# Kernel tuning notes

Measured on AMD Instinct MI355X. Metric: run time of the kernel, lower is better.

## Reference

```python
import jax, jax.numpy as jnp
import numpy as np

B, S, H, E, K = 4, 2048, 1024, 8, 2


def setup_inputs() -> dict:
    key = jax.random.key(0)
    k0, k1, k2 = jax.random.split(key, 3)
    x = jax.random.normal(k0, (B, S, H), dtype=jnp.float32)
    # gate: Linear(H -> E); torch stores W as [out,in], we keep [E,H]
    gate_w = jax.random.normal(k1, (E, H), dtype=jnp.float32) * 0.02
    gate_b = jnp.zeros((E,), dtype=jnp.float32)
    # experts: E x Linear(H -> H); stored as [E, H_in, H_out]
    expert_w = jax.random.normal(k2, (E, H, H), dtype=jnp.float32) * 0.02
    expert_b = jnp.zeros((E, H), dtype=jnp.float32)
    return {"x": x, "gate_w": gate_w, "gate_b": gate_b,
            "expert_w": expert_w, "expert_b": expert_b}


def reference(x, gate_w, gate_b, expert_w, expert_b):
    bsz, seq_len, h = x.shape
    xt = x.reshape(-1, h)                      # [T, H]
    T = xt.shape[0]

    # router (moe_router): softmax -> top-k -> renormalize
    logits = xt @ gate_w.T + gate_b            # [T, E]
    routing_probs = jax.nn.softmax(logits, axis=-1)
    top_k_probs, top_k_index = jax.lax.top_k(routing_probs, K)
    top_k_probs = top_k_probs / jnp.sum(top_k_probs, axis=1, keepdims=True)
    top_k_probs = top_k_probs.astype(x.dtype)

    # combine weights: scatter normalized top-k probs into [T, E]
    rows = jnp.arange(T)[:, None]
    combine = jnp.zeros((T, E), dtype=x.dtype).at[rows, top_k_index].add(top_k_probs)

    # per-expert FFN over all tokens, then weighted combine
    # (equivalent math to the gather / index_add loop: zero weights contribute zero)
    y = jnp.einsum('th,eho->teo', xt, expert_w) + expert_b[None, :, :]  # [T, E, H]
    out = jnp.einsum('te,teh->th', combine, y)                          # [T, H]

    final_output = out.reshape(bsz, seq_len, h)
    return final_output, top_k_index, routing_probs
```

## Files before the change

### kernel.cpp

```cpp
#include <hip/hip_runtime.h>
#include <hip/hip_bf16.h>
#include <stdint.h>

typedef unsigned short ushort_t;
typedef __bf16 bf16x8 __attribute__((ext_vector_type(8)));
typedef float f32x4 __attribute__((ext_vector_type(4)));

#define T_TOK 8192
#define H_DIM 1024
#define E_EXP 8
#define BM 256
#define BN 256
#define BK 64
#define NKT (H_DIM / BK)
#define NITER (NKT / 2)
#define NWG_G 512

#define CNT_STRIDE 64
#define RTOK 32
#define RBLOCKS (T_TOK / RTOK)
#define TP_BLOCKS ((H_DIM / 32) * (H_DIM / 32) * E_EXP)

static __device__ __forceinline__ ushort_t f2bf(float f) {
  union { float f; uint32_t u; } c; c.f = f;
  uint32_t u = c.u;
  uint32_t r = u + 0x7FFFu + ((u >> 16) & 1u);
  return (ushort_t)(r >> 16);
}

__global__ __launch_bounds__(256) void router_transpose(
    const float* __restrict__ x, const float* __restrict__ gw,
    const float* __restrict__ gb, const float* __restrict__ ew,
    float* __restrict__ out_idx, float* __restrict__ out_probs,
    ushort_t* __restrict__ x_bf, int* __restrict__ counts,
    int* __restrict__ tok, float* __restrict__ wts, int* __restrict__ slotmap,
    ushort_t* __restrict__ wT)
{
  __shared__ int   sm_eid[RTOK * 2];
  __shared__ float sm_wt[RTOK * 2];
  __shared__ int   lcnt[E_EXP], lbase[E_EXP], lpos[E_EXP];
  __shared__ float tile[32][33];

  const int tid = threadIdx.x;

  if (blockIdx.x >= RBLOCKS) {
    const int tb = blockIdx.x - RBLOCKS;
    const int e = tb >> 10;
    const int n0 = (tb & 31) * 32, k0 = ((tb >> 5) & 31) * 32;
    const float* we = ew + (size_t)e * H_DIM * H_DIM;
    ushort_t* wTe = wT + (size_t)e * H_DIM * H_DIM;
    const int tx = tid & 31, ty = tid >> 5;
#pragma unroll
    for (int i = 0; i < 4; i++)
      tile[ty + 8 * i][tx] = we[(size_t)(k0 + ty + 8 * i) * H_DIM + n0 + tx];
    __syncthreads();
#pragma unroll
    for (int i = 0; i < 4; i++)
      wTe[(size_t)(n0 + ty + 8 * i) * H_DIM + k0 + tx] = f2bf(tile[tx][ty + 8 * i]);
    return;
  }

  const int wave = tid >> 6, l = tid & 63;
  if (tid < E_EXP) { lcnt[tid] = 0; lpos[tid] = 0; }
  __syncthreads();

  const int t0 = blockIdx.x * RTOK;
  for (int it = 0; it < RTOK / 4; it++) {
    const int lt = wave * (RTOK / 4) + it;
    const int t = t0 + lt;
    const float* xt = x + (size_t)t * H_DIM;
    float acc[E_EXP];
#pragma unroll
    for (int e = 0; e < E_EXP; e++) acc[e] = 0.f;
#pragma unroll
    for (int i = 0; i < 4; i++) {
      const int h = (i * 64 + l) * 4;
      const float4 xv = *reinterpret_cast<const float4*>(xt + h);
      ushort4 b;
      b.x = f2bf(xv.x); b.y = f2bf(xv.y); b.z = f2bf(xv.z); b.w = f2bf(xv.w);
      *reinterpret_cast<ushort4*>(x_bf + (size_t)t * H_DIM + h) = b;
#pragma unroll
      for (int e = 0; e < E_EXP; e++) {
        const float4 g = *reinterpret_cast<const float4*>(gw + e * H_DIM + h);
        acc[e] += xv.x * g.x + xv.y * g.y + xv.z * g.z + xv.w * g.w;
      }
    }
#pragma unroll
    for (int e = 0; e < E_EXP; e++) {
      float v = acc[e];
#pragma unroll
      for (int off = 32; off; off >>= 1) v += __shfl_xor(v, off);
      acc[e] = v;
    }
    if (l == 0) {
      float lg[E_EXP], pb[E_EXP];
      float m = -1e30f;
#pragma unroll
      for (int e = 0; e < E_EXP; e++) { lg[e] = acc[e] + gb[e]; m = fmaxf(m, lg[e]); }
      float s = 0.f;
#pragma unroll
      for (int e = 0; e < E_EXP; e++) { pb[e] = expf(lg[e] - m); s += pb[e]; }
      const float inv = 1.f / s;
#pragma unroll
      for (int e = 0; e < E_EXP; e++) {
        pb[e] *= inv;
        out_probs[(size_t)t * E_EXP + e] = pb[e];
      }
      int i0 = 0; float p0 = pb[0];
#pragma unroll
      for (int e = 1; e < E_EXP; e++) if (pb[e] > p0) { p0 = pb[e]; i0 = e; }
      int i1 = -1; float p1 = -1.f;
#pragma unroll
      for (int e = 0; e < E_EXP; e++) if (e != i0 && pb[e] > p1) { p1 = pb[e]; i1 = e; }
      out_idx[(size_t)t * 2 + 0] = (float)i0;
      out_idx[(size_t)t * 2 + 1] = (float)i1;
      const float rn = 1.f / (p0 + p1);
      sm_eid[lt * 2 + 0] = i0; sm_wt[lt * 2 + 0] = p0 * rn;
      sm_eid[lt * 2 + 1] = i1; sm_wt[lt * 2 + 1] = p1 * rn;
    }
  }
  __syncthreads();

  if (tid < RTOK * 2) atomicAdd(&lcnt[sm_eid[tid]], 1);
  __syncthreads();
  if (tid < E_EXP) lbase[tid] = atomicAdd(&counts[tid * CNT_STRIDE], lcnt[tid]);
  __syncthreads();
  if (tid < RTOK * 2) {
    const int e = sm_eid[tid];
    const int p = lbase[e] + atomicAdd(&lpos[e], 1);
    tok[e * T_TOK + p] = t0 + (tid >> 1);
    wts[e * T_TOK + p] = sm_wt[tid];
    slotmap[(t0 + (tid >> 1)) * 2 + (tid & 1)] = e * T_TOK + p;
  }
}

#define GLDS16(gp, lp)                                                         \
  __builtin_amdgcn_global_load_lds(                                            \
      (const __attribute__((address_space(1))) void*)(gp),                     \
      (__attribute__((address_space(3))) void*)(lp), 16, 0, 0)

#define WAITV6() asm volatile("s_waitcnt vmcnt(6)" ::: "memory")
#define WAITV0() asm volatile("s_waitcnt vmcnt(0)" ::: "memory")
#define LGKM0()                                                                \
  do {                                                                         \
    asm volatile("s_waitcnt lgkmcnt(0)" ::: "memory");                         \
    __builtin_amdgcn_sched_barrier(0);                                         \
  } while (0)
#define BAR()                                                                  \
  do {                                                                         \
    __builtin_amdgcn_sched_barrier(0);                                         \
    __builtin_amdgcn_s_barrier();                                              \
    __builtin_amdgcn_sched_barrier(0);                                         \
  } while (0)

__global__ __launch_bounds__(512, 2) void moe_gemm(
    const ushort_t* __restrict__ x_bf, const ushort_t* __restrict__ wT,
    const float* __restrict__ bias, const int* __restrict__ counts,
    const int* __restrict__ tok, const float* __restrict__ wts,
    ushort_t* __restrict__ y)
{
  __shared__ __align__(16) ushort_t AsR[2 * 2 * BM * 32];
  __shared__ __align__(16) ushort_t BsR[2 * 2 * BM * 32];
  __shared__ int stok[BM];
  __shared__ float swt[BM];
#define AS_(buf, kh, idx) AsR[((buf) * 2 + (kh)) * 8192 + (idx)]
#define BS_(buf, kh, idx) BsR[((buf) * 2 + (kh)) * 8192 + (idx)]

  const int tid = threadIdx.x;
  const int bid = blockIdx.x;

  int ne[E_EXP], fl[E_EXP];
  int bulk_total = 0;
#pragma unroll
  for (int i = 0; i < E_EXP; i++) {
    ne[i] = counts[i * CNT_STRIDE];
    fl[i] = ne[i] >> 8;
    bulk_total += fl[i] * 4;
  }

  if (bid < bulk_total) {
    int e = 0, local = bid, done = 0;
#pragma unroll
    for (int i = 0; i < E_EXP; i++) {
      const int sz = fl[i] * 4;
      if (!done) { if (local < sz) { e = i; done = 1; } else local -= sz; }
    }
    const int mt = local >> 2;
    const int nt = local & 3;

    if (tid < BM) {
      stok[tid] = tok[e * T_TOK + mt * BM + tid];
      swt[tid] = wts[e * T_TOK + mt * BM + tid];
    }
    __syncthreads();

    const int r0 = tid >> 2;
    const int cp = (tid & 3) ^ ((tid >> 3) & 3);
    const ushort_t* wTe = wT + (size_t)e * H_DIM * H_DIM;
    const ushort_t* aP0 = x_bf + (size_t)stok[r0] * H_DIM + cp * 8;
    const ushort_t* aP1 = x_bf + (size_t)stok[r0 + 128] * H_DIM + cp * 8;
    const ushort_t* bP0 = wTe + (size_t)(nt * BN + r0) * H_DIM + cp * 8;
    const ushort_t* bP1 = wTe + (size_t)(nt * BN + r0 + 128) * H_DIM + cp * 8;
    const int d0 = tid * 8;
    const int d1 = (tid + 512) * 8;

#define STAGE_A(t, kh, buf)                                                    \
  do {                                                                         \
    GLDS16(aP0 + (t) * BK + (kh) * 32, &AS_((buf), (kh), d0));                 \
    GLDS16(aP1 + (t) * BK + (kh) * 32, &AS_((buf), (kh), d1));                 \
  } while (0)
#define STAGE_B(t, kh, buf)                                                    \
  do {                                                                         \
    GLDS16(bP0 + (t) * BK + (kh) * 32, &BS_((buf), (kh), d0));                 \
    GLDS16(bP1 + (t) * BK + (kh) * 32, &BS_((buf), (kh), d1));                 \
  } while (0)

    const int l = tid & 63;
    const int wid = tid >> 6;
    const int wm = wid >> 2, wn = wid & 3;
    const int fr = l & 15;
    const int g = l >> 4;
    const int sl = g ^ ((l >> 1) & 3);
    const int arow0 = wm * 128 + fr;
    const int brow0 = wn * 64 + fr;

    bf16x8 af[8], bv[2];
    f32x4 acc[8][4] = {};

#define READ_A(buf, kk)                                                        \
  do {                                                                         \
    _Pragma("unroll") for (int mi = 0; mi < 8; mi++)                           \
        af[mi] = *reinterpret_cast<const bf16x8*>(                             \
            &AS_((buf), (kk), (arow0 + mi * 16) * 32 + sl * 8));               \
  } while (0)
#define READ_B(buf, kk, nh)                                                    \
  do {                                                                         \
    _Pragma("unroll") for (int j = 0; j < 2; j++)                              \
        bv[j] = *reinterpret_cast<const bf16x8*>(                              \
            &BS_((buf), (kk), (brow0 + ((nh) * 2 + j) * 16) * 32 + sl * 8));   \
  } while (0)
#define MFMA16(nh)                                                             \
  do {                                                                         \
    __builtin_amdgcn_s_setprio(1);                                             \
    _Pragma("unroll") for (int mi = 0; mi < 8; mi++)                           \
        _Pragma("unroll") for (int j = 0; j < 2; j++)                          \
            acc[mi][(nh) * 2 + j] = __builtin_amdgcn_mfma_f32_16x16x32_bf16(   \
                af[mi], bv[j], acc[mi][(nh) * 2 + j], 0, 0, 0);                \
    __builtin_amdgcn_s_setprio(0);                                             \
  } while (0)

#define ITER_BODY(TT, MORE)                                                    \
  do {                                                                         \
                                                                       \
    READ_A(0, 0); READ_B(0, 0, 0);                                             \
    STAGE_B((TT) + 1, 1, 1);                                                   \
    BAR(); LGKM0(); MFMA16(0); BAR();                                          \
                                                                       \
    READ_B(0, 0, 1);                                                           \
    if (MORE) STAGE_A((TT) + 2, 0, 0);                                         \
    BAR(); LGKM0(); MFMA16(1); BAR();                                          \
                                                                       \
    READ_A(0, 1); READ_B(0, 1, 0);                                             \
    if (MORE) STAGE_B((TT) + 2, 0, 0);                                         \
    BAR(); LGKM0(); MFMA16(0); BAR();                                          \
                                               \
    READ_B(0, 1, 1);                                                           \
    if (MORE) { STAGE_A((TT) + 2, 1, 0); WAITV6(); } else { WAITV0(); }        \
    BAR(); LGKM0(); MFMA16(1); BAR();                                          \
                                                                       \
    READ_A(1, 0); READ_B(1, 0, 0);                                             \
    if (MORE) STAGE_B((TT) + 2, 1, 0);                                         \
    BAR(); LGKM0(); MFMA16(0); BAR();                                          \
                                                                       \
    READ_B(1, 0, 1);                                                           \
    if (MORE) STAGE_A((TT) + 3, 0, 1);                                         \
    BAR(); LGKM0(); MFMA16(1); BAR();                                          \
                                                                       \
    READ_A(1, 1); READ_B(1, 1, 0);                                             \
    if (MORE) STAGE_B((TT) + 3, 0, 1);                                         \
    BAR(); LGKM0(); MFMA16(0); BAR();                                          \
                                               \
    READ_B(1, 1, 1);                                                           \
    if (MORE) { STAGE_A((TT) + 3, 1, 1); WAITV6(); }                           \
    BAR(); LGKM0(); MFMA16(1); BAR();                                          \
  } while (0)

    STAGE_A(0, 0, 0); STAGE_B(0, 0, 0); STAGE_A(0, 1, 0); STAGE_B(0, 1, 0);
    STAGE_A(1, 0, 1); STAGE_B(1, 0, 1); STAGE_A(1, 1, 1);
    WAITV6();
    BAR();

#pragma unroll 1
    for (int it = 0; it < NITER - 1; ++it) {
      const int t = 2 * it;
      ITER_BODY(t, 1);
    }
    {
      const int t = 2 * (NITER - 1);
      ITER_BODY(t, 0);
    }

    ushort_t* ye = y + ((size_t)e * T_TOK + (size_t)mt * BM) * H_DIM;
    float bias4[4];
#pragma unroll
    for (int nj = 0; nj < 4; nj++)
      bias4[nj] = bias[e * H_DIM + nt * BN + wn * 64 + nj * 16 + fr];
#pragma unroll
    for (int mi = 0; mi < 8; mi++) {
      const int rr0 = wm * 128 + mi * 16 + g * 4;
#pragma unroll
      for (int r = 0; r < 4; r++) {
        const int row = rr0 + r;
        const float wgt = swt[row];
#pragma unroll
        for (int nj = 0; nj < 4; nj++) {
          const int n = nt * BN + wn * 64 + nj * 16 + fr;
          ye[(size_t)row * H_DIM + n] = f2bf(wgt * (acc[mi][nj][r] + bias4[nj]));
        }
      }
    }
    return;
  }

  {
    const int tb0 = bid - bulk_total;
    int tc[E_EXP];
    int tail_total = 0;
#pragma unroll
    for (int i = 0; i < E_EXP; i++) {
      const int rem = ne[i] - (fl[i] << 8);
      tc[i] = (rem + 63) >> 6;
      tail_total += tc[i] * 8;
    }
    if (tb0 >= tail_total) return;
    int e = 0, local = tb0, done = 0;
#pragma unroll
    for (int i = 0; i < E_EXP; i++) {
      const int sz = tc[i] * 8;
      if (!done) { if (local < sz) { e = i; done = 1; } else local -= sz; }
    }
    const int mtt = local >> 3;
    const int ntt = local & 7;
    const int row0 = (fl[e] << 8) + mtt * 64;
    int valid = ne[e] - row0; if (valid > 64) valid = 64;

    if (tid < 64) {
      int slot = row0 + tid;
      if (slot >= ne[e]) slot = ne[e] - 1;
      stok[tid] = tok[e * T_TOK + slot];
      swt[tid] = wts[e * T_TOK + slot];
    }
    __syncthreads();

    const ushort_t* wTe = wT + (size_t)e * H_DIM * H_DIM;
    const int trow = tid >> 3;
    const int tlc = (tid & 7) ^ (trow & 7);
    const ushort_t* taS = x_bf + (size_t)stok[trow] * H_DIM + tlc * 8;
    const ushort_t* tbS0 = wTe + (size_t)(ntt * 128 + trow) * H_DIM + tlc * 8;
    const ushort_t* tbS1 = tbS0 + (size_t)64 * H_DIM;

#define TSTAGE(t, buf)                                                         \
  do {                                                                         \
    GLDS16(taS + (t) * BK, &AsR[(buf) * 4096 + tid * 8]);                      \
    GLDS16(tbS0 + (t) * BK, &BsR[(buf) * 8192 + tid * 8]);                     \
    GLDS16(tbS1 + (t) * BK, &BsR[(buf) * 8192 + (tid + 512) * 8]);             \
  } while (0)

    const int l = tid & 63;
    const int wid = tid >> 6;
    const int fr = l & 15;
    const int g = l >> 4;
    const int tph0 = (g ^ (fr & 7)) * 8;
    const int tph1 = ((4 ^ g) ^ (fr & 7)) * 8;

    f32x4 tacc[4] = {};

    TSTAGE(0, 0);
    WAITV0();
    BAR();

#pragma unroll
    for (int t = 0; t < NKT; ++t) {
      if (t + 1 < NKT) TSTAGE(t + 1, (t + 1) & 1);
      const ushort_t* Ab = &AsR[(t & 1) * 4096];
      const ushort_t* Bb = &BsR[(t & 1) * 8192];
#pragma unroll
      for (int kk = 0; kk < 2; kk++) {
        const int ph = kk ? tph1 : tph0;
        const bf16x8 tbv = *reinterpret_cast<const bf16x8*>(
            &Bb[(wid * 16 + fr) * 64 + ph]);
#pragma unroll
        for (int mi = 0; mi < 4; mi++) {
          const bf16x8 tav = *reinterpret_cast<const bf16x8*>(
              &Ab[(mi * 16 + fr) * 64 + ph]);
          tacc[mi] = __builtin_amdgcn_mfma_f32_16x16x32_bf16(
              tav, tbv, tacc[mi], 0, 0, 0);
        }
      }
      WAITV0();
      BAR();
    }

    ushort_t* ye = y + ((size_t)e * T_TOK + row0) * H_DIM;
    const int ncol = ntt * 128 + wid * 16 + fr;
    const float bs = bias[e * H_DIM + ncol];
#pragma unroll
    for (int mi = 0; mi < 4; mi++) {
      const int rb = mi * 16 + g * 4;
#pragma unroll
      for (int r = 0; r < 4; r++) {
        const int row = rb + r;
        if (row < valid) {
          ye[(size_t)row * H_DIM + ncol] = f2bf(swt[row] * (tacc[mi][r] + bs));
        }
      }
    }
  }
}

__global__ __launch_bounds__(256) void combine_kernel(
    const ushort_t* __restrict__ y, const int* __restrict__ slotmap,
    float* __restrict__ out)
{
  const int t = blockIdx.x;
  const int s0 = slotmap[t * 2 + 0];
  const int s1 = slotmap[t * 2 + 1];
  const ushort_t* r0 = y + (size_t)s0 * H_DIM;
  const ushort_t* r1 = y + (size_t)s1 * H_DIM;
  float* o = out + (size_t)t * H_DIM;
  const int h = threadIdx.x * 4;
  const ushort4 u0 = *reinterpret_cast<const ushort4*>(r0 + h);
  const ushort4 u1 = *reinterpret_cast<const ushort4*>(r1 + h);
  float4 v;
  union { uint32_t u; float f; } c;
  c.u = (uint32_t)u0.x << 16; v.x = c.f; c.u = (uint32_t)u1.x << 16; v.x += c.f;
  c.u = (uint32_t)u0.y << 16; v.y = c.f; c.u = (uint32_t)u1.y << 16; v.y += c.f;
  c.u = (uint32_t)u0.z << 16; v.z = c.f; c.u = (uint32_t)u1.z << 16; v.z += c.f;
  c.u = (uint32_t)u0.w << 16; v.w = c.f; c.u = (uint32_t)u1.w << 16; v.w += c.f;
  *reinterpret_cast<float4*>(o + h) = v;
}

extern "C" void kernel_launch(void* const* d_in, const int* in_sizes, int n_in,
                              void* d_out, int out_size, void* d_ws, size_t ws_size,
                              hipStream_t stream)
{
  const float* x  = (const float*)d_in[0];
  const float* gw = (const float*)d_in[1];
  const float* gb = (const float*)d_in[2];
  const float* ew = (const float*)d_in[3];
  const float* eb = (const float*)d_in[4];

  float* out = (float*)d_out;
  float* out_final = out;
  float* out_idx   = out + (size_t)T_TOK * H_DIM;
  float* out_probs = out_idx + (size_t)T_TOK * 2;

  char* ws = (char*)d_ws;
  size_t off = 0;
  int*      counts  = (int*)(ws + off); off += 4096;
  int*      tok     = (int*)(ws + off); off += (size_t)E_EXP * T_TOK * 4;
  float*    wts     = (float*)(ws + off); off += (size_t)E_EXP * T_TOK * 4;
  int*      slotmap = (int*)(ws + off); off += (size_t)T_TOK * 2 * 4;
  ushort_t* x_bf    = (ushort_t*)(ws + off); off += (size_t)T_TOK * H_DIM * 2;
  ushort_t* wT      = (ushort_t*)(ws + off); off += (size_t)E_EXP * H_DIM * H_DIM * 2;
  ushort_t* y       = (ushort_t*)(ws + off); off += (size_t)E_EXP * T_TOK * H_DIM * 2;

  hipMemsetAsync(counts, 0, 4096, stream);

  router_transpose<<<RBLOCKS + TP_BLOCKS, 256, 0, stream>>>(
      x, gw, gb, ew, out_idx, out_probs, x_bf, counts, tok, wts, slotmap, wT);
  moe_gemm<<<NWG_G, 512, 0, stream>>>(x_bf, wT, eb, counts, tok, wts, y);
  combine_kernel<<<T_TOK, 256, 0, stream>>>(y, slotmap, out_final);
}
```

Baseline: 97.30 us.

## Switch MoE GEMM to persistent workgroups with XCD-affine atomic work queues

Replaces the static one-tile-per-workgroup grid with a persistent kernel of 256 workgroups that pull tiles from per-expert atomic counters, preferring the expert matching their XCD index so each expert's weights stay in one XCD's L2. Once those queues drain, workgroups steal from other experts and then take tail tiles from a shared counter. This targets load imbalance and L2 locality for weight reads. The cost is extra atomics and barriers per tile, and the queue counters in the counts buffer must be zeroed before each launch; that reset is not visible here.

Result: slower. 126.2 us (+29.7%).

```diff
diff --git a/kernel.cpp b/kernel.cpp
--- a/kernel.cpp
+++ b/kernel.cpp
@@ -14,7 +14,7 @@
 #define BK 64
 #define NKT (H_DIM / BK)
 #define NITER (NKT / 2)
-#define NWG_G 512
+#define NWG_G 256
 
 #define CNT_STRIDE 64
 #define RTOK 32
@@ -155,7 +155,7 @@
 
 __global__ __launch_bounds__(512, 2) void moe_gemm(
     const ushort_t* __restrict__ x_bf, const ushort_t* __restrict__ wT,
-    const float* __restrict__ bias, const int* __restrict__ counts,
+    const float* __restrict__ bias, int* __restrict__ counts,
     const int* __restrict__ tok, const float* __restrict__ wts,
     ushort_t* __restrict__ y)
 {
@@ -163,46 +163,71 @@
   __shared__ __align__(16) ushort_t BsR[2 * 2 * BM * 32];
   __shared__ int stok[BM];
   __shared__ float swt[BM];
+  __shared__ int s_q, s_e, s_kind;
 #define AS_(buf, kh, idx) AsR[((buf) * 2 + (kh)) * 8192 + (idx)]
 #define BS_(buf, kh, idx) BsR[((buf) * 2 + (kh)) * 8192 + (idx)]
 
   const int tid = threadIdx.x;
-  const int bid = blockIdx.x;
-
-  int ne[E_EXP], fl[E_EXP];
-  int bulk_total = 0;
+  const int xcd = blockIdx.x & 7;
+
+  int ne[E_EXP], fl[E_EXP], tc[E_EXP];
+  int tail_total = 0;
 #pragma unroll
   for (int i = 0; i < E_EXP; i++) {
     ne[i] = counts[i * CNT_STRIDE];
     fl[i] = ne[i] >> 8;
-    bulk_total += fl[i] * 4;
+    tc[i] = ((ne[i] - (fl[i] << 8)) + 63) >> 6;
+    tail_total += tc[i] * 8;
   }
-
-  if (bid < bulk_total) {
-    int e = 0, local = bid, done = 0;
-#pragma unroll
-    for (int i = 0; i < E_EXP; i++) {
-      const int sz = fl[i] * 4;
-      if (!done) { if (local < sz) { e = i; done = 1; } else local -= sz; }
-    }
-    const int mt = local >> 2;
-    const int nt = local & 3;
-
-    if (tid < BM) {
-      stok[tid] = tok[e * T_TOK + mt * BM + tid];
-      swt[tid] = wts[e * T_TOK + mt * BM + tid];
+  int* qb = counts + 512;
+  int* qt = counts + 512 + 8 * 16;
+
+  const int l = tid & 63;
+  const int wid = tid >> 6;
+  const int fr = l & 15;
+  const int g = l >> 4;
+
+  for (;;) {
+    __syncthreads();
+    if (tid == 0) {
+      int q = -1, te = -1, kind = 0;
+      for (int dx = 0; dx < E_EXP && q < 0; ++dx) {
+        const int x2 = (xcd + dx) & 7;
+        const int lim = fl[x2] * 4;
+        if (lim > 0) {
+          const int c = atomicAdd(&qb[x2 * 16], 1);
+          if (c < lim) { q = c; te = x2; }
+        }
+      }
+      if (q < 0) {
+        const int c = atomicAdd(qt, 1);
+        if (c < tail_total) { q = c; kind = 1; }
+      }
+      s_q = q; s_e = te; s_kind = kind;
     }
     __syncthreads();
-
-    const int r0 = tid >> 2;
-    const int cp = (tid & 3) ^ ((tid >> 3) & 3);
-    const ushort_t* wTe = wT + (size_t)e * H_DIM * H_DIM;
-    const ushort_t* aP0 = x_bf + (size_t)stok[r0] * H_DIM + cp * 8;
-    const ushort_t* aP1 = x_bf + (size_t)stok[r0 + 128] * H_DIM + cp * 8;
-    const ushort_t* bP0 = wTe + (size_t)(nt * BN + r0) * H_DIM + cp * 8;
-    const ushort_t* bP1 = wTe + (size_t)(nt * BN + r0 + 128) * H_DIM + cp * 8;
-    const int d0 = tid * 8;
-    const int d1 = (tid + 512) * 8;
+    if (s_q < 0) break;
+
+    if (s_kind == 0) {
+      const int e = s_e;
+      const int mt = s_q >> 2;
+      const int nt = s_q & 3;
+
+      if (tid < BM) {
+        stok[tid] = tok[e * T_TOK + mt * BM + tid];
+        swt[tid] = wts[e * T_TOK + mt * BM + tid];
+      }
+      __syncthreads();
+
+      const int r0 = tid >> 2;
+      const int cp = (tid & 3) ^ ((tid >> 3) & 3);
+      const ushort_t* wTe = wT + (size_t)e * H_DIM * H_DIM;
+      const ushort_t* aP0 = x_bf + (size_t)stok[r0] * H_DIM + cp * 8;
+      const ushort_t* aP1 = x_bf + (size_t)stok[r0 + 128] * H_DIM + cp * 8;
+      const ushort_t* bP0 = wTe + (size_t)(nt * BN + r0) * H_DIM + cp * 8;
+      const ushort_t* bP1 = wTe + (size_t)(nt * BN + r0 + 128) * H_DIM + cp * 8;
+      const int d0 = tid * 8;
+      const int d1 = (tid + 512) * 8;
 
 #define STAGE_A(t, kh, buf)                                                    \
   do {                                                                         \
@@ -215,17 +240,13 @@
     GLDS16(bP1 + (t) * BK + (kh) * 32, &BS_((buf), (kh), d1));                 \
   } while (0)
 
-    const int l = tid & 63;
-    const int wid = tid >> 6;
-    const int wm = wid >> 2, wn = wid & 3;
-    const int fr = l & 15;
-    const int g = l >> 4;
-    const int sl = g ^ ((l >> 1) & 3);
-    const int arow0 = wm * 128 + fr;
-    const int brow0 = wn * 64 + fr;
-
-    bf16x8 af[8], bv[2];
-    f32x4 acc[8][4] = {};
+      const int wm = wid >> 2, wn = wid & 3;
+      const int sl = g ^ ((l >> 1) & 3);
+      const int arow0 = wm * 128 + fr;
+      const int brow0 = wn * 64 + fr;
+
+      bf16x8 af[8], bv[2];
+      f32x4 acc[8][4] = {};
 
 #define READ_A(buf, kk)                                                        \
   do {                                                                         \
@@ -285,79 +306,66 @@
     BAR(); LGKM0(); MFMA16(1); BAR();                                          \
   } while (0)
 
-    STAGE_A(0, 0, 0); STAGE_B(0, 0, 0); STAGE_A(0, 1, 0); STAGE_B(0, 1, 0);
-    STAGE_A(1, 0, 1); STAGE_B(1, 0, 1); STAGE_A(1, 1, 1);
-    WAITV6();
-    BAR();
+      STAGE_A(0, 0, 0); STAGE_B(0, 0, 0); STAGE_A(0, 1, 0); STAGE_B(0, 1, 0);
+      STAGE_A(1, 0, 1); STAGE_B(1, 0, 1); STAGE_A(1, 1, 1);
+      WAITV6();
+      BAR();
 
 #pragma unroll 1
-    for (int it = 0; it < NITER - 1; ++it) {
-      const int t = 2 * it;
-      ITER_BODY(t, 1);
-    }
-    {
-      const int t = 2 * (NITER - 1);
-      ITER_BODY(t, 0);
-    }
-
-    ushort_t* ye = y + ((size_t)e * T_TOK + (size_t)mt * BM) * H_DIM;
-    float bias4[4];
-#pragma unroll
-    for (int nj = 0; nj < 4; nj++)
-      bias4[nj] = bias[e * H_DIM + nt * BN + wn * 64 + nj * 16 + fr];
-#pragma unroll
-    for (int mi = 0; mi < 8; mi++) {
-      const int rr0 = wm * 128 + mi * 16 + g * 4;
-#pragma unroll
-      for (int r = 0; r < 4; r++) {
-        const int row = rr0 + r;
-        const float wgt = swt[row];
-#pragma unroll
-        for (int nj = 0; nj < 4; nj++) {
-          const int n = nt * BN + wn * 64 + nj * 16 + fr;
-          ye[(size_t)row * H_DIM + n] = f2bf(wgt * (acc[mi][nj][r] + bias4[nj]));
+      for (int it = 0; it < NITER - 1; ++it) {
+        const int t = 2 * it;
+        ITER_BODY(t, 1);
+      }
+      {
+        const int t = 2 * (NITER - 1);
+        ITER_BODY(t, 0);
+      }
+
+      ushort_t* ye = y + ((size_t)e * T_TOK + (size_t)mt * BM) * H_DIM;
+      float bias4[4];
+#pragma unroll
+      for (int nj = 0; nj < 4; nj++)
+        bias4[nj] = bias[e * H_DIM + nt * BN + wn * 64 + nj * 16 + fr];
+#pragma unroll
+      for (int mi = 0; mi < 8; mi++) {
+        const int rr0 = wm * 128 + mi * 16 + g * 4;
+#pragma unroll
+        for (int r = 0; r < 4; r++) {
+          const int row = rr0 + r;
+          const float wgt = swt[row];
+#pragma unroll
+          for (int nj = 0; nj < 4; nj++) {
+            const int n = nt * BN + wn * 64 + nj * 16 + fr;
+            ye[(size_t)row * H_DIM + n] = f2bf(wgt * (acc[mi][nj][r] + bias4[nj]));
+          }
         }
       }
-    }
-    return;
-  }
-
-  {
-    const int tb0 = bid - bulk_total;
-    int tc[E_EXP];
-    int tail_total = 0;
-#pragma unroll
-    for (int i = 0; i < E_EXP; i++) {
-      const int rem = ne[i] - (fl[i] << 8);
-      tc[i] = (rem + 63) >> 6;
-      tail_total += tc[i] * 8;
-    }
-    if (tb0 >= tail_total) return;
-    int e = 0, local = tb0, done = 0;
-#pragma unroll
-    for (int i = 0; i < E_EXP; i++) {
-      const int sz = tc[i] * 8;
-      if (!done) { if (local < sz) { e = i; done = 1; } else local -= sz; }
-    }
-    const int mtt = local >> 3;
-    const int ntt = local & 7;
-    const int row0 = (fl[e] << 8) + mtt * 64;
-    int valid = ne[e] - row0; if (valid > 64) valid = 64;
-
-    if (tid < 64) {
-      int slot = row0 + tid;
-      if (slot >= ne[e]) slot = ne[e] - 1;
-      stok[tid] = tok[e * T_TOK + slot];
-      swt[tid] = wts[e * T_TOK + slot];
-    }
-    __syncthreads();
-
-    const ushort_t* wTe = wT + (size_t)e * H_DIM * H_DIM;
-    const int trow = tid >> 3;
-    const int tlc = (tid & 7) ^ (trow & 7);
-    const ushort_t* taS = x_bf + (size_t)stok[trow] * H_DIM + tlc * 8;
-    const ushort_t* tbS0 = wTe + (size_t)(ntt * 128 + trow) * H_DIM + tlc * 8;
-    const ushort_t* tbS1 = tbS0 + (size_t)64 * H_DIM;
+    } else {
+      int e = 0, local = s_q, done = 0;
+#pragma unroll
+      for (int i = 0; i < E_EXP; i++) {
+        const int sz = tc[i] * 8;
+        if (!done) { if (local < sz) { e = i; done = 1; } else local -= sz; }
+      }
+      const int mtt = local >> 3;
+      const int ntt = local & 7;
+      const int row0 = (fl[e] << 8) + mtt * 64;
+      int valid = ne[e] - row0; if (valid > 64) valid = 64;
+
+      if (tid < 64) {
+        int slot = row0 + tid;
+        if (slot >= ne[e]) slot = ne[e] - 1;
+        stok[tid] = tok[e * T_TOK + slot];
+        swt[tid] = wts[e * T_TOK + slot];
+      }
+      __syncthreads();
+
+      const ushort_t* wTe = wT + (size_t)e * H_DIM * H_DIM;
+      const int trow = tid >> 3;
+      const int tlc = (tid & 7) ^ (trow & 7);
+      const ushort_t* taS = x_bf + (size_t)stok[trow] * H_DIM + tlc * 8;
+      const ushort_t* tbS0 = wTe + (size_t)(ntt * 128 + trow) * H_DIM + tlc * 8;
+      const ushort_t* tbS1 = tbS0 + (size_t)64 * H_DIM;
 
 #define TSTAGE(t, buf)                                                         \
   do {                                                                         \
@@ -366,52 +374,49 @@
     GLDS16(tbS1 + (t) * BK, &BsR[(buf) * 8192 + (tid + 512) * 8]);             \
   } while (0)
 
-    const int l = tid & 63;
-    const int wid = tid >> 6;
-    const int fr = l & 15;
-    const int g = l >> 4;
-    const int tph0 = (g ^ (fr & 7)) * 8;
-    const int tph1 = ((4 ^ g) ^ (fr & 7)) * 8;
-
-    f32x4 tacc[4] = {};
-
-    TSTAGE(0, 0);
-    WAITV0();
-    BAR();
-
-#pragma unroll
-    for (int t = 0; t < NKT; ++t) {
-      if (t + 1 < NKT) TSTAGE(t + 1, (t + 1) & 1);
-      const ushort_t* Ab = &AsR[(t & 1) * 4096];
-      const ushort_t* Bb = &BsR[(t & 1) * 8192];
-#pragma unroll
-      for (int kk = 0; kk < 2; kk++) {
-        const int ph = kk ? tph1 : tph0;
-        const bf16x8 tbv = *reinterpret_cast<const bf16x8*>(
-            &Bb[(wid * 16 + fr) * 64 + ph]);
-#pragma unroll
-        for (int mi = 0; mi < 4; mi++) {
-          const bf16x8 tav = *reinterpret_cast<const bf16x8*>(
-              &Ab[(mi * 16 + fr) * 64 + ph]);
-          tacc[mi] = __builtin_amdgcn_mfma_f32_16x16x32_bf16(
-              tav, tbv, tacc[mi], 0, 0, 0);
-        }
-      }
+      const int tph0 = (g ^ (fr & 7)) * 8;
+      const int tph1 = ((4 ^ g) ^ (fr & 7)) * 8;
+
+      f32x4 tacc[4] = {};
+
+      TSTAGE(0, 0);
       WAITV0();
       BAR();
-    }
-
-    ushort_t* ye = y + ((size_t)e * T_TOK + row0) * H_DIM;
-    const int ncol = ntt * 128 + wid * 16 + fr;
-    const float bs = bias[e * H_DIM + ncol];
-#pragma unroll
-    for (int mi = 0; mi < 4; mi++) {
-      const int rb = mi * 16 + g * 4;
-#pragma unroll
-      for (int r = 0; r < 4; r++) {
-        const int row = rb + r;
-        if (row < valid) {
-          ye[(size_t)row * H_DIM + ncol] = f2bf(swt[row] * (tacc[mi][r] + bs));
+
+#pragma unroll
+      for (int t = 0; t < NKT; ++t) {
+        if (t + 1 < NKT) TSTAGE(t + 1, (t + 1) & 1);
+        const ushort_t* Ab = &AsR[(t & 1) * 4096];
+        const ushort_t* Bb = &BsR[(t & 1) * 8192];
+#pragma unroll
+        for (int kk = 0; kk < 2; kk++) {
+          const int ph = kk ? tph1 : tph0;
+          const bf16x8 tbv = *reinterpret_cast<const bf16x8*>(
+              &Bb[(wid * 16 + fr) * 64 + ph]);
+#pragma unroll
+          for (int mi = 0; mi < 4; mi++) {
+            const bf16x8 tav = *reinterpret_cast<const bf16x8*>(
+                &Ab[(mi * 16 + fr) * 64 + ph]);
+            tacc[mi] = __builtin_amdgcn_mfma_f32_16x16x32_bf16(
+                tav, tbv, tacc[mi], 0, 0, 0);
+          }
+        }
+        WAITV0();
+        BAR();
+      }
+
+      ushort_t* ye = y + ((size_t)e * T_TOK + row0) * H_DIM;
+      const int ncol = ntt * 128 + wid * 16 + fr;
+      const float bs = bias[e * H_DIM + ncol];
+#pragma unroll
+      for (int mi = 0; mi < 4; mi++) {
+        const int rb = mi * 16 + g * 4;
+#pragma unroll
+        for (int r = 0; r < 4; r++) {
+          const int row = rb + r;
+          if (row < valid) {
+            ye[(size_t)row * H_DIM + ncol] = f2bf(swt[row] * (tacc[mi][r] + bs));
+          }
         }
       }
     }
```

## Interleave expert tiles across blocks with atomic spill assignment for overloaded experts

Applied to the files above, without the earlier changes.

Replaces the prefix-sum mapping of block index to (expert, tile) with a fixed interleaved mapping: the first 256 blocks give each expert up to 32 home bulk tiles, with bid&7 selecting the expert. Extra tiles for overloaded experts are claimed dynamically through an atomic counter in the counts buffer. Tail blocks are likewise indexed per expert by bid&7. The intent is to spread experts evenly across blocks so that neighbouring workgroups share expert weights and load stays balanced. In exchange it relies on a counter at counts[520] that must be zeroed before each launch, and on the launch grid being large enough to cover this fixed layout.

Result: faster. 95.11 us (-2.3%).

```diff
diff --git a/kernel.cpp b/kernel.cpp
--- a/kernel.cpp
+++ b/kernel.cpp
@@ -155,7 +155,7 @@
 
 __global__ __launch_bounds__(512, 2) void moe_gemm(
     const ushort_t* __restrict__ x_bf, const ushort_t* __restrict__ wT,
-    const float* __restrict__ bias, const int* __restrict__ counts,
+    const float* __restrict__ bias, int* __restrict__ counts,
     const int* __restrict__ tok, const float* __restrict__ wts,
     ushort_t* __restrict__ y)
 {
@@ -163,6 +163,7 @@
   __shared__ __align__(16) ushort_t BsR[2 * 2 * BM * 32];
   __shared__ int stok[BM];
   __shared__ float swt[BM];
+  __shared__ int s_spill;
 #define AS_(buf, kh, idx) AsR[((buf) * 2 + (kh)) * 8192 + (idx)]
 #define BS_(buf, kh, idx) BsR[((buf) * 2 + (kh)) * 8192 + (idx)]
 
@@ -170,23 +171,42 @@
   const int bid = blockIdx.x;
 
   int ne[E_EXP], fl[E_EXP];
-  int bulk_total = 0;
 #pragma unroll
   for (int i = 0; i < E_EXP; i++) {
     ne[i] = counts[i * CNT_STRIDE];
     fl[i] = ne[i] >> 8;
-    bulk_total += fl[i] * 4;
   }
 
-  if (bid < bulk_total) {
-    int e = 0, local = bid, done = 0;
-#pragma unroll
-    for (int i = 0; i < E_EXP; i++) {
-      const int sz = fl[i] * 4;
-      if (!done) { if (local < sz) { e = i; done = 1; } else local -= sz; }
-    }
-    const int mt = local >> 2;
-    const int nt = local & 3;
+  const int l = tid & 63;
+  const int wid = tid >> 6;
+  const int fr = l & 15;
+  const int g = l >> 4;
+
+  if (bid < 256) {
+    int e = bid & 7;
+    int q = bid >> 3;
+    const int home = fl[e] * 4;
+    if (q >= (home < 32 ? home : 32)) {
+      int sc[E_EXP], spill_total = 0;
+#pragma unroll
+      for (int i = 0; i < E_EXP; i++) {
+        sc[i] = fl[i] * 4 > 32 ? fl[i] * 4 - 32 : 0;
+        spill_total += sc[i];
+      }
+      if (spill_total == 0) return;
+      if (tid == 0) s_spill = atomicAdd(&counts[520], 1);
+      __syncthreads();
+      int k = s_spill;
+      if (k >= spill_total) return;
+      int done = 0;
+#pragma unroll
+      for (int i = 0; i < E_EXP; i++) {
+        if (!done) { if (k < sc[i]) { e = i; done = 1; } else k -= sc[i]; }
+      }
+      q = 32 + k;
+    }
+    const int mt = q >> 2;
+    const int nt = q & 3;
 
     if (tid < BM) {
       stok[tid] = tok[e * T_TOK + mt * BM + tid];
@@ -215,11 +235,7 @@
     GLDS16(bP1 + (t) * BK + (kh) * 32, &BS_((buf), (kh), d1));                 \
   } while (0)
 
-    const int l = tid & 63;
-    const int wid = tid >> 6;
     const int wm = wid >> 2, wn = wid & 3;
-    const int fr = l & 15;
-    const int g = l >> 4;
     const int sl = g ^ ((l >> 1) & 3);
     const int arow0 = wm * 128 + fr;
     const int brow0 = wn * 64 + fr;
@@ -319,28 +335,14 @@
         }
       }
     }
-    return;
-  }
-
-  {
-    const int tb0 = bid - bulk_total;
-    int tc[E_EXP];
-    int tail_total = 0;
-#pragma unroll
-    for (int i = 0; i < E_EXP; i++) {
-      const int rem = ne[i] - (fl[i] << 8);
-      tc[i] = (rem + 63) >> 6;
-      tail_total += tc[i] * 8;
-    }
-    if (tb0 >= tail_total) return;
-    int e = 0, local = tb0, done = 0;
-#pragma unroll
-    for (int i = 0; i < E_EXP; i++) {
-      const int sz = tc[i] * 8;
-      if (!done) { if (local < sz) { e = i; done = 1; } else local -= sz; }
-    }
-    const int mtt = local >> 3;
-    const int ntt = local & 7;
+  } else {
+    const int e = bid & 7;
+    const int tq = (bid - 256) >> 3;
+    const int rem = ne[e] - (fl[e] << 8);
+    const int tcnt = (rem + 63) >> 6;
+    if (tq >= tcnt * 8) return;
+    const int mtt = tq >> 3;
+    const int ntt = tq & 7;
     const int row0 = (fl[e] << 8) + mtt * 64;
     int valid = ne[e] - row0; if (valid > 64) valid = 64;
 
@@ -366,10 +368,6 @@
     GLDS16(tbS1 + (t) * BK, &BsR[(buf) * 8192 + (tid + 512) * 8]);             \
   } while (0)
 
-    const int l = tid & 63;
-    const int wid = tid >> 6;
-    const int fr = l & 15;
-    const int g = l >> 4;
     const int tph0 = (g ^ (fr & 7)) * 8;
     const int tph1 = ((4 ^ g) ^ (fr & 7)) * 8;
 
```
